# Kernel optimization log

Measured on AMD Instinct MI355X. Metric: run time of the kernel, lower is better.

The kernel has to match this reference:

```python
import jax, jax.numpy as jnp
import numpy as np

N = 50000      # nodes
IN = 256       # in_feat
H = 4          # num_heads
DH = 64        # out_feat // num_heads
R = 6          # number of relations
E = 300000     # edges per relation
NEG_SLOPE = 0.2  # DGL GATConv leaky_relu slope


def setup_inputs() -> dict:
    key = jax.random.key(0)
    ks = jax.random.split(key, 7)
    x = jax.random.normal(ks[0], (N, IN), dtype=jnp.float32)
    W = jax.random.normal(ks[1], (R, IN, H * DH), dtype=jnp.float32) * (1.0 / np.sqrt(IN))
    attn_l = jax.random.normal(ks[2], (R, H, DH), dtype=jnp.float32) * 0.1
    attn_r = jax.random.normal(ks[3], (R, H, DH), dtype=jnp.float32) * 0.1
    bias = jax.random.normal(ks[4], (R, H * DH), dtype=jnp.float32) * 0.01
    src = jax.random.randint(ks[5], (R, E), 0, N, dtype=jnp.int32).astype(jnp.int64)
    dst = jax.random.randint(ks[6], (R, E), 0, N, dtype=jnp.int32).astype(jnp.int64)
    return {"x": x, "W": W, "attn_l": attn_l, "attn_r": attn_r, "bias": bias,
            "src": src, "dst": dst}


def reference(x, W, attn_l, attn_r, bias, src, dst):
    n = x.shape[0]
    r_total, h, dh = attn_l.shape
    out = jnp.zeros((n, h, dh), dtype=x.dtype)
    # small fixed loop over structurally-distinct relations (HeteroGraphConv)
    for r in range(r_total):
        feat = (x @ W[r]).reshape(n, h, dh)            # [N,H,Dh] shared src/dst proj
        el = jnp.sum(feat * attn_l[r], axis=-1)        # [N,H]
        er = jnp.sum(feat * attn_r[r], axis=-1)        # [N,H]
        s, d = src[r], dst[r]
        e = jax.nn.leaky_relu(el[s] + er[d], NEG_SLOPE)  # [E,H]
        # segmented softmax over incoming edges of each dst node
        m = jax.ops.segment_max(e, d, num_segments=n)    # [N,H]
        m = jnp.where(jnp.isfinite(m), m, 0.0)
        a = jnp.exp(e - m[d])                            # [E,H]
        z = jax.ops.segment_sum(a, d, num_segments=n)    # [N,H]
        alpha = a / jnp.maximum(z[d], 1e-9)              # [E,H]
        msg = alpha[:, :, None] * feat[s]                # [E,H,Dh]
        agg = jax.ops.segment_sum(msg, d, num_segments=n)  # [N,H,Dh]
        # GATConv: bias + activation(relu) per relation, HeteroGraphConv sums
        out = out + jax.nn.relu(agg + bias[r].reshape(h, dh))
    hcat = out.reshape(n, h * dh)                        # merge='cat' view
    return jax.nn.relu(hcat)                             # layer-level activation
```

## Files before the change

### kernel.cpp

```cpp
#include <hip/hip_runtime.h>

#define NN 50000
#define MP 50048
#define NH 4
#define NR 6
#define NE 300000
#define HD 256
#define SLOTS 32
#define NB 512
#define BSZ ((NE + NB - 1) / NB)

typedef __attribute__((ext_vector_type(4))) float f32x4;
typedef __attribute__((ext_vector_type(8))) short bf16x8;

__device__ __forceinline__ short f2bf(float f) {
  unsigned u = __float_as_uint(f);
  unsigned r = (u + 0x7FFFu + ((u >> 16) & 1u)) >> 16;
  return (short)r;
}
__device__ __forceinline__ float bf2f_lo(unsigned d) {
  return __uint_as_float(d << 16);
}
__device__ __forceinline__ float bf2f_hi(unsigned d) {
  return __uint_as_float(d & 0xffff0000u);
}

#define GLOAD_LDS16(g, l)                                                     \
  __builtin_amdgcn_global_load_lds(                                           \
      (const __attribute__((address_space(1))) void*)(g),                     \
      (__attribute__((address_space(3))) void*)(l), 16, 0, 0)

__global__ __launch_bounds__(256) void cast_x_kernel(
    const float* __restrict__ x, short* __restrict__ xb, int n4) {
  const int i = blockIdx.x * 256 + threadIdx.x;
  if (i >= n4) return;
  const float4 v = ((const float4*)x)[i];
  short4 o;
  o.x = f2bf(v.x); o.y = f2bf(v.y); o.z = f2bf(v.z); o.w = f2bf(v.w);
  ((short4*)xb)[i] = o;
}

__global__ __launch_bounds__(256) void cast_wt_kernel(
    const float* __restrict__ W, short* __restrict__ wt) {
  __shared__ float ts[32][33];
  const int bx = blockIdx.x;
  const int r = bx >> 6;
  const int tile = bx & 63;
  const int k0 = (tile >> 3) * 32;
  const int n0 = (tile & 7) * 32;
  const int t = threadIdx.x;
  const int col = t & 31;
  const int rr = t >> 5;
#pragma unroll
  for (int p = 0; p < 4; ++p) {
    const int row = p * 8 + rr;
    ts[row][col] = W[(size_t)r * 65536 + (k0 + row) * 256 + n0 + col];
  }
  __syncthreads();
#pragma unroll
  for (int p = 0; p < 4; ++p) {
    const int row = p * 8 + rr;
    wt[(size_t)r * 65536 + (n0 + row) * 256 + k0 + col] = f2bf(ts[col][row]);
  }
}

__global__ __launch_bounds__(256) void gemm_kernel(
    const short* __restrict__ xb,
    const short* __restrict__ wt_all,
    const float* __restrict__ attn_l,
    const float* __restrict__ attn_r,
    short* __restrict__ featb_all,
    float* __restrict__ el_all, float* __restrict__ er_all) {
  __shared__ short As[128 * 64];
  __shared__ short Bs[128 * 64];
  const int t = threadIdx.x;
  const int lane = t & 63;
  const int w = t >> 6;
  const int wm = w & 1, wn = w >> 1;
  const int row0 = blockIdx.x * 128;
  const int n0 = blockIdx.y * 128;
  const int r = blockIdx.z;
  const short* wt = wt_all + (size_t)r * 65536;
  short* featb = featb_all + (size_t)r * MP * 256;

  f32x4 acc[4][4];
#pragma unroll
  for (int mi = 0; mi < 4; ++mi)
#pragma unroll
    for (int ni = 0; ni < 4; ++ni) {
      f32x4 z = {0.f, 0.f, 0.f, 0.f};
      acc[mi][ni] = z;
    }

  const short* ag[4];
  const short* bg[4];
  short* la[4];
  short* lb[4];
#pragma unroll
  for (int i = 0; i < 4; ++i) {
    const int c = t + 256 * i;
    const int row = c >> 3;
    const int sslot = (c & 7) ^ (row & 7);
    int ar = row0 + row; if (ar >= NN) ar = NN - 1;
    ag[i] = xb + (size_t)ar * 256 + sslot * 8;
    bg[i] = wt + (size_t)(n0 + row) * 256 + sslot * 8;
    la[i] = As + c * 8;
    lb[i] = Bs + c * 8;
  }

  const int ra = lane & 15;
  const int qg = lane >> 4;

  for (int k0 = 0; k0 < 256; k0 += 64) {
#pragma unroll
    for (int i = 0; i < 4; ++i) {
      GLOAD_LDS16(ag[i] + k0, la[i]);
      GLOAD_LDS16(bg[i] + k0, lb[i]);
    }
    __syncthreads();
#pragma unroll
    for (int kk = 0; kk < 2; ++kk) {
      bf16x8 af[4], bfr[4];
#pragma unroll
      for (int mi = 0; mi < 4; ++mi) {
        const int rw = wm * 64 + mi * 16 + ra;
        const int ch = (kk * 4 + qg) ^ (rw & 7);
        af[mi] = *(const bf16x8*)&As[rw * 64 + ch * 8];
      }
#pragma unroll
      for (int ni = 0; ni < 4; ++ni) {
        const int rw = wn * 64 + ni * 16 + ra;
        const int ch = (kk * 4 + qg) ^ (rw & 7);
        bfr[ni] = *(const bf16x8*)&Bs[rw * 64 + ch * 8];
      }
#pragma unroll
      for (int mi = 0; mi < 4; ++mi)
#pragma unroll
        for (int ni = 0; ni < 4; ++ni)
          acc[mi][ni] = __builtin_amdgcn_mfma_f32_16x16x32_bf16(
              af[mi], bfr[ni], acc[mi][ni], 0, 0, 0);
    }
    __syncthreads();
  }

  const int h = (n0 >> 6) + wn;
  float alv[4], arv[4];
#pragma unroll
  for (int ni = 0; ni < 4; ++ni) {
    alv[ni] = attn_l[r * HD + h * 64 + ni * 16 + ra];
    arv[ni] = attn_r[r * HD + h * 64 + ni * 16 + ra];
  }
#pragma unroll
  for (int mi = 0; mi < 4; ++mi) {
#pragma unroll
    for (int j = 0; j < 4; ++j) {
      const int row = row0 + wm * 64 + mi * 16 + (lane >> 4) * 4 + j;
      float elp = 0.f, erp = 0.f;
#pragma unroll
      for (int ni = 0; ni < 4; ++ni) {
        const float v = acc[mi][ni][j];
        featb[(size_t)row * 256 + n0 + wn * 64 + ni * 16 + ra] = f2bf(v);
        elp = fmaf(v, alv[ni], elp);
        erp = fmaf(v, arv[ni], erp);
      }
#pragma unroll
      for (int m = 1; m < 16; m <<= 1) {
        elp += __shfl_xor(elp, m, 64);
        erp += __shfl_xor(erp, m, 64);
      }
      if (ra == 0 && row < NN) {
        el_all[((size_t)r * NN + row) * NH + h] = elp;
        er_all[((size_t)r * NN + row) * NH + h] = erp;
      }
    }
  }
}

__global__ __launch_bounds__(256) void build_kernel(
    const int* __restrict__ src, const int* __restrict__ dst,
    int* __restrict__ deg, unsigned short* __restrict__ slots) {
  const int lo = blockIdx.x * BSZ;
  const int hi = (lo + BSZ < NE) ? lo + BSZ : NE;
  for (int r = 0; r < NR; ++r) {
    for (int i = lo + threadIdx.x; i < hi; i += 256) {
      const int s = src[(size_t)r * NE + i];
      const int d = dst[(size_t)r * NE + i];
      const int g = r * NN + d;
      const int sl = atomicAdd(&deg[g], 1);
      if (sl < SLOTS)
        slots[(size_t)g * SLOTS + sl] = (unsigned short)s;
    }
  }
}

__global__ __launch_bounds__(256) void agg_kernel(
    const short* __restrict__ featb_all, const float* __restrict__ el_all,
    const float* __restrict__ er_all, const int* __restrict__ deg,
    const unsigned short* __restrict__ slots, const float* __restrict__ bias,
    float* __restrict__ out) {
  const int wid = (blockIdx.x * 256 + threadIdx.x) >> 6;
  const int lane = threadIdx.x & 63;
  if (wid >= NN) return;
  const int h = lane >> 4;
  const int c0 = lane * 4;

  float oacc[4] = {0.f, 0.f, 0.f, 0.f};
  const int wid_u = __builtin_amdgcn_readfirstlane(wid);

  const int g_first = (NR - 1) * NN + wid_u;
  const uint4* spf = (const uint4*)(slots + (size_t)g_first * SLOTS);
  uint4 sq0 = spf[0], sq1 = spf[1], sq2 = spf[2], sq3 = spf[3];
  int dgv = deg[g_first];
  float erv = er_all[(size_t)g_first * NH + h];

  for (int r = NR - 1; r >= 0; --r) {
    const int dg0 = __builtin_amdgcn_readfirstlane(dgv);
    const int dg = dg0 > SLOTS ? SLOTS : dg0;
    unsigned sdv[16];
    sdv[0]  = __builtin_amdgcn_readfirstlane(sq0.x);
    sdv[1]  = __builtin_amdgcn_readfirstlane(sq0.y);
    sdv[2]  = __builtin_amdgcn_readfirstlane(sq0.z);
    sdv[3]  = __builtin_amdgcn_readfirstlane(sq0.w);
    sdv[4]  = __builtin_amdgcn_readfirstlane(sq1.x);
    sdv[5]  = __builtin_amdgcn_readfirstlane(sq1.y);
    sdv[6]  = __builtin_amdgcn_readfirstlane(sq1.z);
    sdv[7]  = __builtin_amdgcn_readfirstlane(sq1.w);
    sdv[8]  = __builtin_amdgcn_readfirstlane(sq2.x);
    sdv[9]  = __builtin_amdgcn_readfirstlane(sq2.y);
    sdv[10] = __builtin_amdgcn_readfirstlane(sq2.z);
    sdv[11] = __builtin_amdgcn_readfirstlane(sq2.w);
    sdv[12] = __builtin_amdgcn_readfirstlane(sq3.x);
    sdv[13] = __builtin_amdgcn_readfirstlane(sq3.y);
    sdv[14] = __builtin_amdgcn_readfirstlane(sq3.z);
    sdv[15] = __builtin_amdgcn_readfirstlane(sq3.w);
    const float er_nh = erv;

    if (r > 0) {
      const int g2 = (r - 1) * NN + wid_u;
      const uint4* sp2 = (const uint4*)(slots + (size_t)g2 * SLOTS);
      sq0 = sp2[0]; sq1 = sp2[1]; sq2 = sp2[2]; sq3 = sp2[3];
      dgv = deg[g2];
      erv = er_all[(size_t)g2 * NH + h];
    }

    const float* elr = el_all + (size_t)r * NN * NH;
    const short* fb = featb_all + (size_t)r * MP * 256;

    float z = 0.f;
    float acc[4] = {0.f, 0.f, 0.f, 0.f};

#pragma unroll
    for (int j0 = 0; j0 < SLOTS; j0 += 8) {
      if (j0 >= dg) break;
      float pv[8];
      uint2 rw[8];
#pragma unroll
      for (int k = 0; k < 8; ++k) {
        const int e = j0 + k;
        int s = (int)((e & 1) ? (sdv[e >> 1] >> 16) : (sdv[e >> 1] & 0xffffu));
        const bool v = e < dg;
        s = v ? s : 0;
        rw[k] = *(const uint2*)(fb + (size_t)s * 256 + c0);
        float ev = elr[s * NH + h] + er_nh;
        ev = fmaxf(ev, 0.2f * ev);
        pv[k] = v ? __expf(ev) : 0.f;
      }
#pragma unroll
      for (int k = 0; k < 8; ++k) {
        z += pv[k];
        acc[0] = fmaf(pv[k], bf2f_lo(rw[k].x), acc[0]);
        acc[1] = fmaf(pv[k], bf2f_hi(rw[k].x), acc[1]);
        acc[2] = fmaf(pv[k], bf2f_lo(rw[k].y), acc[2]);
        acc[3] = fmaf(pv[k], bf2f_hi(rw[k].y), acc[3]);
      }
    }

    const float inv = 1.f / fmaxf(z, 1e-9f);
    const float4 bv = *(const float4*)(bias + r * HD + c0);
    oacc[0] += fmaxf(fmaf(acc[0], inv, bv.x), 0.f);
    oacc[1] += fmaxf(fmaf(acc[1], inv, bv.y), 0.f);
    oacc[2] += fmaxf(fmaf(acc[2], inv, bv.z), 0.f);
    oacc[3] += fmaxf(fmaf(acc[3], inv, bv.w), 0.f);
  }

  float4 o4 = {oacc[0], oacc[1], oacc[2], oacc[3]};
  *(float4*)(out + (size_t)wid * 256 + c0) = o4;
}

extern "C" void kernel_launch(void* const* d_in, const int* in_sizes, int n_in,
                              void* d_out, int out_size, void* d_ws,
                              size_t ws_size, hipStream_t stream) {
  const float* x      = (const float*)d_in[0];
  const float* W      = (const float*)d_in[1];
  const float* attn_l = (const float*)d_in[2];
  const float* attn_r = (const float*)d_in[3];
  const float* bias   = (const float*)d_in[4];
  const int*   src    = (const int*)d_in[5];
  const int*   dst    = (const int*)d_in[6];
  float* out = (float*)d_out;

  char* p = (char*)d_ws;
  auto alloc = [&](size_t bytes) {
    char* r = p;
    p += (bytes + 255) & ~(size_t)255;
    return r;
  };
  short* xb    = (short*)alloc((size_t)NN * HD * 2);
  short* wt    = (short*)alloc((size_t)NR * 256 * 256 * 2);
  short* featb = (short*)alloc((size_t)NR * MP * 256 * 2);
  float* el    = (float*)alloc((size_t)NR * NN * NH * 4);
  float* er    = (float*)alloc((size_t)NR * NN * NH * 4);
  int*   deg   = (int*)alloc((size_t)NR * NN * 4);
  unsigned short* slots =
      (unsigned short*)alloc((size_t)NR * NN * SLOTS * 2);

  hipMemsetAsync(deg, 0, (size_t)NR * NN * 4, stream);

  cast_x_kernel<<<(NN * HD / 4 + 255) / 256, 256, 0, stream>>>(x, xb,
                                                               NN * HD / 4);
  cast_wt_kernel<<<NR * 64, 256, 0, stream>>>(W, wt);
  build_kernel<<<NB, 256, 0, stream>>>(src, dst, deg, slots);
  gemm_kernel<<<dim3(MP / 128, 2, NR), 256, 0, stream>>>(xb, wt, attn_l,
                                                         attn_r, featb, el,
                                                         er);
  agg_kernel<<<(NN * 64) / 256, 256, 0, stream>>>(featb, el, er, deg, slots,
                                                  bias, out);
}
```

Baseline: 466.0 us.

## Compute attention logits via precomputed W·attn projection in separate GEMM

Folds attn_l/attn_r into the weight matrix (W·a) so el/er become a small x @ [256x48] GEMM in a new kernel, removing the dot-product and shuffle-reduction epilogue from the main projection GEMM. The main GEMM now only writes bf16 features. This adds two extra launches and a second pass over x, and rounds the folded weights to bf16, which changes numerics slightly.

```diff
diff --git a/kernel.cpp b/kernel.cpp
--- a/kernel.cpp
+++ b/kernel.cpp
@@ -64,13 +64,118 @@
   }
 }
 
+__global__ __launch_bounds__(256) void wlwr_kernel(
+    const float* __restrict__ W, const float* __restrict__ attn_l,
+    const float* __restrict__ attn_r, short* __restrict__ wlwr) {
+  const int idx = blockIdx.x * 256 + threadIdx.x;
+  if (idx >= 128 * 256) return;
+  const int k = idx & 255;
+  const int n = idx >> 8;
+  float v = 0.f;
+  if (n < 48) {
+    const int r = n >> 3, h = (n >> 1) & 3, side = n & 1;
+    const float* a = (side ? attn_r : attn_l) + r * 256 + h * 64;
+    const float* wrow = W + (size_t)r * 65536 + (size_t)k * 256 + h * 64;
+#pragma unroll 8
+    for (int dh = 0; dh < 64; ++dh) v = fmaf(wrow[dh], a[dh], v);
+  }
+  wlwr[(size_t)n * 256 + k] = f2bf(v);
+}
+
+__global__ __launch_bounds__(256) void eler_kernel(
+    const short* __restrict__ xb, const short* __restrict__ wlwr,
+    float* __restrict__ el_all, float* __restrict__ er_all) {
+  __shared__ short As[128 * 64];
+  __shared__ short Bs[128 * 64];
+  const int t = threadIdx.x;
+  const int lane = t & 63;
+  const int w = t >> 6;
+  const int wm = w & 1, wn = w >> 1;
+  const int row0 = blockIdx.x * 128;
+
+  f32x4 acc[4][4];
+#pragma unroll
+  for (int mi = 0; mi < 4; ++mi)
+#pragma unroll
+    for (int ni = 0; ni < 4; ++ni) {
+      f32x4 z = {0.f, 0.f, 0.f, 0.f};
+      acc[mi][ni] = z;
+    }
+
+  const short* ag[4];
+  const short* bg[4];
+  short* la[4];
+  short* lb[4];
+#pragma unroll
+  for (int i = 0; i < 4; ++i) {
+    const int c = t + 256 * i;
+    const int row = c >> 3;
+    const int sslot = (c & 7) ^ (row & 7);
+    int ar = row0 + row; if (ar >= NN) ar = NN - 1;
+    ag[i] = xb + (size_t)ar * 256 + sslot * 8;
+    bg[i] = wlwr + (size_t)row * 256 + sslot * 8;
+    la[i] = As + c * 8;
+    lb[i] = Bs + c * 8;
+  }
+
+  const int ra = lane & 15;
+  const int qg = lane >> 4;
+
+  for (int k0 = 0; k0 < 256; k0 += 64) {
+#pragma unroll
+    for (int i = 0; i < 4; ++i) {
+      GLOAD_LDS16(ag[i] + k0, la[i]);
+      GLOAD_LDS16(bg[i] + k0, lb[i]);
+    }
+    __syncthreads();
+#pragma unroll
+    for (int kk = 0; kk < 2; ++kk) {
+      bf16x8 af[4], bfr[4];
+#pragma unroll
+      for (int mi = 0; mi < 4; ++mi) {
+        const int rw = wm * 64 + mi * 16 + ra;
+        const int ch = (kk * 4 + qg) ^ (rw & 7);
+        af[mi] = *(const bf16x8*)&As[rw * 64 + ch * 8];
+      }
+#pragma unroll
+      for (int ni = 0; ni < 4; ++ni) {
+        const int rw = wn * 64 + ni * 16 + ra;
+        const int ch = (kk * 4 + qg) ^ (rw & 7);
+        bfr[ni] = *(const bf16x8*)&Bs[rw * 64 + ch * 8];
+      }
+#pragma unroll
+      for (int mi = 0; mi < 4; ++mi)
+#pragma unroll
+        for (int ni = 0; ni < 4; ++ni)
+          acc[mi][ni] = __builtin_amdgcn_mfma_f32_16x16x32_bf16(
+              af[mi], bfr[ni], acc[mi][ni], 0, 0, 0);
+    }
+    __syncthreads();
+  }
+
+#pragma unroll
+  for (int mi = 0; mi < 4; ++mi) {
+#pragma unroll
+    for (int j = 0; j < 4; ++j) {
+      const int row = row0 + wm * 64 + mi * 16 + (lane >> 4) * 4 + j;
+      if (row >= NN) continue;
+#pragma unroll
+      for (int ni = 0; ni < 4; ++ni) {
+        const int c = wn * 64 + ni * 16 + ra;
+        if (c < 48) {
+          const int r = c >> 3, h = (c >> 1) & 3, side = c & 1;
+          float* dstp = (side ? er_all : el_all);
+          dstp[((size_t)r * NN + row) * NH + h] = acc[mi][ni][j];
+        }
+      }
+    }
+  }
+}
+
 __global__ __launch_bounds__(256) void gemm_kernel(
     const short* __restrict__ xb,
     const short* __restrict__ wt_all,
-    const float* __restrict__ attn_l,
-    const float* __restrict__ attn_r,
-    short* __restrict__ featb_all,
-    float* __restrict__ el_all, float* __restrict__ er_all) {
+    short* __restrict__ featb_all) {
   __shared__ short As[128 * 64];
   __shared__ short Bs[128 * 64];
   const int t = threadIdx.x;
@@ -143,35 +248,15 @@
     __syncthreads();
   }
 
-  const int h = (n0 >> 6) + wn;
-  float alv[4], arv[4];
-#pragma unroll
-  for (int ni = 0; ni < 4; ++ni) {
-    alv[ni] = attn_l[r * HD + h * 64 + ni * 16 + ra];
-    arv[ni] = attn_r[r * HD + h * 64 + ni * 16 + ra];
-  }
 #pragma unroll
   for (int mi = 0; mi < 4; ++mi) {
 #pragma unroll
     for (int j = 0; j < 4; ++j) {
       const int row = row0 + wm * 64 + mi * 16 + (lane >> 4) * 4 + j;
-      float elp = 0.f, erp = 0.f;
-#pragma unroll
-      for (int ni = 0; ni < 4; ++ni) {
-        const float v = acc[mi][ni][j];
-        featb[(size_t)row * 256 + n0 + wn * 64 + ni * 16 + ra] = f2bf(v);
-        elp = fmaf(v, alv[ni], elp);
-        erp = fmaf(v, arv[ni], erp);
-      }
-#pragma unroll
-      for (int m = 1; m < 16; m <<= 1) {
-        elp += __shfl_xor(elp, m, 64);
-        erp += __shfl_xor(erp, m, 64);
-      }
-      if (ra == 0 && row < NN) {
-        el_all[((size_t)r * NN + row) * NH + h] = elp;
-        er_all[((size_t)r * NN + row) * NH + h] = erp;
-      }
+#pragma unroll
+      for (int ni = 0; ni < 4; ++ni)
+        featb[(size_t)row * 256 + n0 + wn * 64 + ni * 16 + ra] =
+            f2bf(acc[mi][ni][j]);
     }
   }
 }
@@ -307,6 +392,7 @@
   };
   short* xb    = (short*)alloc((size_t)NN * HD * 2);
   short* wt    = (short*)alloc((size_t)NR * 256 * 256 * 2);
+  short* wlwr  = (short*)alloc((size_t)128 * 256 * 2);
   short* featb = (short*)alloc((size_t)NR * MP * 256 * 2);
   float* el    = (float*)alloc((size_t)NR * NN * NH * 4);
   float* er    = (float*)alloc((size_t)NR * NN * NH * 4);
@@ -319,10 +405,10 @@
   cast_x_kernel<<<(NN * HD / 4 + 255) / 256, 256, 0, stream>>>(x, xb,
                                                                NN * HD / 4);
   cast_wt_kernel<<<NR * 64, 256, 0, stream>>>(W, wt);
+  wlwr_kernel<<<128, 256, 0, stream>>>(W, attn_l, attn_r, wlwr);
   build_kernel<<<NB, 256, 0, stream>>>(src, dst, deg, slots);
-  gemm_kernel<<<dim3(MP / 128, 2, NR), 256, 0, stream>>>(xb, wt, attn_l,
-                                                         attn_r, featb, el,
-                                                         er);
+  eler_kernel<<<MP / 128, 256, 0, stream>>>(xb, wlwr, el, er);
+  gemm_kernel<<<dim3(MP / 128, 2, NR), 256, 0, stream>>>(xb, wt, featb);
   agg_kernel<<<(NN * 64) / 256, 256, 0, stream>>>(featb, el, er, deg, slots,
                                                   bias, out);
 }
```

New measurement: 458.2 us. Within noise of the previous version (-1.7%).
